# Kernel tuning notes

Measured on AMD Instinct MI355X. Metric: run time of the kernel, lower is better.

## Reference

```python
import jax, jax.numpy as jnp
import numpy as np

HEADS = 16
DIM_HEAD = 128
SCALE = DIM_HEAD ** -0.5


def rotate_half(x):
    # x: (..., d) with d even; pairs (x1, x2) -> (-x2, x1)
    x = x.reshape(*x.shape[:-1], -1, 2)
    x1, x2 = x[..., 0], x[..., 1]
    return jnp.stack([-x2, x1], axis=-1).reshape(*x.shape[:-2], -1)


def apply_rotary(freqs, t):
    # freqs: (n, d), t: (b, h, n, d)
    cos = jnp.cos(freqs)[None, None]
    sin = jnp.sin(freqs)[None, None]
    return t * cos + rotate_half(t) * sin


def setup_inputs() -> dict:
    key = jax.random.key(0)
    ks = jax.random.split(key, 6)
    b, n, dim = 2, 2048, 2048
    inner = HEADS * DIM_HEAD
    s = dim ** -0.5
    x = jax.random.normal(ks[0], (b, n, dim), dtype=jnp.float32)
    rotary_emb = jax.random.normal(ks[1], (n, DIM_HEAD), dtype=jnp.float32)
    Wq = jax.random.normal(ks[2], (dim, inner), dtype=jnp.float32) * s
    Wkv = jax.random.normal(ks[3], (dim, 2 * inner), dtype=jnp.float32) * s
    Wo = jax.random.normal(ks[4], (inner, dim), dtype=jnp.float32) * s
    bo = jnp.zeros((dim,), dtype=jnp.float32)
    return {"x": x, "rotary_emb": rotary_emb, "Wq": Wq, "Wkv": Wkv, "Wo": Wo, "bo": bo}


def reference(x, rotary_emb, Wq, Wkv, Wo, bo):
    b, n, _ = x.shape
    q = x @ Wq                      # (b, n, inner)
    kv = x @ Wkv                    # (b, n, 2*inner)
    k, v = jnp.split(kv, 2, axis=-1)
    # b n (h d) -> b h n d
    split = lambda t: t.reshape(b, n, HEADS, DIM_HEAD).transpose(0, 2, 1, 3)
    q, k, v = split(q), split(k), split(v)
    q = apply_rotary(rotary_emb, q)
    k = apply_rotary(rotary_emb, k)
    q = q * SCALE
    dots = jnp.einsum('bhid,bhjd->bhij', q, k)
    attn = jax.nn.softmax(dots, axis=-1)
    out = jnp.einsum('bhij,bhjd->bhid', attn, v)
    out = out.transpose(0, 2, 1, 3).reshape(b, n, HEADS * DIM_HEAD)
    return out @ Wo + bo
```

## Files before the change

kernel.cpp:

```cpp
#include <hip/hip_runtime.h>
#include <hip/hip_bf16.h>
#include <stdint.h>

typedef __attribute__((ext_vector_type(8))) short s16x8;
typedef __attribute__((ext_vector_type(4))) float f32x4;

#define DEVFN static __device__ __forceinline__

constexpr int   S_LEN = 2048;
constexpr int   DH    = 128;
constexpr int   INNER = 2048;
constexpr float ASCALE = 0.08838834764831845f;

constexpr float SM_L2E  = 1.44269504f;
constexpr float SM_BIAS = 12.0f * 1.44269504f;

DEVFN unsigned short f2b(float f) {
  union { __hip_bfloat16 h; unsigned short u; } v;
  v.h = __float2bfloat16(f);
  return v.u;
}
DEVFN void async_cp16(const unsigned short* g, unsigned short* l) {
  __builtin_amdgcn_global_load_lds((const __attribute__((address_space(1))) void*)g,
                                   (__attribute__((address_space(3))) void*)l, 16, 0, 0);
}

__global__ __launch_bounds__(256) void cvt_bf16_k(const float* __restrict__ in,
                                                  unsigned short* __restrict__ out) {
  const size_t e = ((size_t)blockIdx.x * 256 + threadIdx.x) * 8;
  const float4 a = *(const float4*)(in + e);
  const float4 b = *(const float4*)(in + e + 4);
  union { s16x8 v; unsigned short u[8]; } o;
  o.u[0] = f2b(a.x); o.u[1] = f2b(a.y); o.u[2] = f2b(a.z); o.u[3] = f2b(a.w);
  o.u[4] = f2b(b.x); o.u[5] = f2b(b.y); o.u[6] = f2b(b.z); o.u[7] = f2b(b.w);
  *(s16x8*)(out + e) = o.v;
}

__global__ __launch_bounds__(256) void rot_cs_k(const float* __restrict__ rot,
                                                float2* __restrict__ cst) {
  const int idx = blockIdx.x * 256 + threadIdx.x;
  const float f = rot[idx];
  float s, c;
  __sincosf(f, &s, &c);
  cst[idx] = make_float2(c, s);
}

__global__ __launch_bounds__(256) void transpose_cvt_k(const float* __restrict__ in,
                                                       unsigned short* __restrict__ out,
                                                       int R, int C) {
  __shared__ __align__(16) unsigned short tile[64][72];
  const int t  = threadIdx.x;
  const int lr = t >> 3;
  const int lc = (t & 7) << 3;
  const size_t ibase = (size_t)blockIdx.y * 64 * C + (size_t)blockIdx.x * 64;
#pragma unroll
  for (int rr = 0; rr < 64; rr += 32) {
    const float* p = in + ibase + (size_t)(rr + lr) * C + lc;
    const float4 a = *(const float4*)p;
    const float4 b = *(const float4*)(p + 4);
    unsigned short* tp = &tile[rr + lr][lc];
    tp[0] = f2b(a.x); tp[1] = f2b(a.y); tp[2] = f2b(a.z); tp[3] = f2b(a.w);
    tp[4] = f2b(b.x); tp[5] = f2b(b.y); tp[6] = f2b(b.z); tp[7] = f2b(b.w);
  }
  __syncthreads();
  const size_t obase = (size_t)blockIdx.x * 64 * R + (size_t)blockIdx.y * 64;
#pragma unroll
  for (int rr = 0; rr < 64; rr += 32) {
    int oc = rr + lr;
    union { s16x8 v; unsigned short s[8]; } u;
#pragma unroll
    for (int j = 0; j < 8; ++j) u.s[j] = tile[lc + j][oc];
    *(s16x8*)(out + obase + (size_t)oc * R + lc) = u.v;
  }
}

__global__ __launch_bounds__(512, 2) void gemm256_qk(
    const unsigned short* __restrict__ A,
    const unsigned short* __restrict__ Bt,
    unsigned short* __restrict__ out0,
    unsigned short* __restrict__ out1,
    const float2* __restrict__ rotcs) {
  constexpr int K = 2048, NT = 32;
  __shared__ __align__(16) unsigned short smem[65536];
  const int tid = threadIdx.x;
  const int wid = tid >> 6, lane = tid & 63;
  const int wm = wid >> 2, wn = wid & 3;
  const int quad = lane >> 4, l15 = lane & 15, l7 = l15 & 7;

  const int lin = blockIdx.x;
  const int logical = (lin & 7) * 32 + (lin >> 3);
  const int m0 = (logical & 15) * 256;
  const int n0 = (logical >> 4) * 256;

  const int r0 = tid >> 3, c0 = tid & 7;

  f32x4 acc[8][4];
#pragma unroll
  for (int i = 0; i < 8; ++i)
#pragma unroll
    for (int j = 0; j < 4; ++j) acc[i][j] = {0.f, 0.f, 0.f, 0.f};

  auto stageA = [&](int t, int h) {
#pragma unroll
    for (int s = 0; s < 2; ++s) {
      const int r = s * 64 + r0;
      async_cp16(A + (size_t)(m0 + h * 128 + r) * K + t * 64 + ((c0 ^ (r0 & 7)) << 3),
                 smem + ((t & 1) * 2 + h) * 8192 + s * 4096 + tid * 8);
    }
  };
  auto stageB = [&](int t, int h) {
#pragma unroll
    for (int s = 0; s < 2; ++s) {
      const int r = s * 64 + r0;
      async_cp16(Bt + (size_t)(n0 + h * 128 + r) * K + t * 64 + ((c0 ^ (r0 & 7)) << 3),
                 smem + 32768 + ((t & 1) * 2 + h) * 8192 + s * 4096 + tid * 8);
    }
  };

  stageA(0, 0); stageA(0, 1); stageB(0, 0); stageB(0, 1);
  stageB(1, 0); stageB(1, 1);
  asm volatile("s_waitcnt vmcnt(4)" ::: "memory");
  __builtin_amdgcn_s_barrier();

#pragma unroll 2
  for (int t = 0; t < NT; ++t) {
    const int cur = t & 1;
    const unsigned short* Ab = smem + (cur * 2 + wm) * 8192;
    const unsigned short* Bb = smem + 32768 + (cur * 2 + (wn >> 1)) * 8192;
    const int bln = (wn & 1) * 64;
    s16x8 bf[4][2];
#pragma unroll
    for (int p = 0; p < 2; ++p) {
      s16x8 af[2][2];
#pragma unroll
      for (int j = 0; j < 2; ++j)
#pragma unroll
        for (int kk = 0; kk < 2; ++kk)
          af[j][kk] = *(const s16x8*)(Ab + ((4 * p + j) * 16 + l15) * 64 + (((kk * 4 + quad) ^ l7) << 3));
      if (p == 0) {
#pragma unroll
        for (int nf = 0; nf < 4; ++nf)
#pragma unroll
          for (int kk = 0; kk < 2; ++kk)
            bf[nf][kk] = *(const s16x8*)(Bb + (bln + nf * 16 + l15) * 64 + (((kk * 4 + quad) ^ l7) << 3));
        if (t + 1 < NT) { stageA(t + 1, 0); stageA(t + 1, 1); }
      } else {
        if (t + 2 < NT) { stageB(t + 2, 0); stageB(t + 2, 1); }
      }
      __builtin_amdgcn_s_barrier();
      asm volatile("s_waitcnt lgkmcnt(0)" ::: "memory");
      s16x8 ag[2][2];
#pragma unroll
      for (int j = 0; j < 2; ++j)
#pragma unroll
        for (int kk = 0; kk < 2; ++kk)
          ag[j][kk] = *(const s16x8*)(Ab + ((4 * p + 2 + j) * 16 + l15) * 64 + (((kk * 4 + quad) ^ l7) << 3));
      __builtin_amdgcn_sched_barrier(0);
      __builtin_amdgcn_s_setprio(1);
#pragma unroll
      for (int kk = 0; kk < 2; ++kk)
#pragma unroll
        for (int j = 0; j < 2; ++j)
#pragma unroll
          for (int nf = 0; nf < 4; ++nf)
            acc[4 * p + j][nf] = __builtin_amdgcn_mfma_f32_16x16x32_bf16(af[j][kk], bf[nf][kk], acc[4 * p + j][nf], 0, 0, 0);
      __builtin_amdgcn_s_setprio(0);
      asm volatile("s_waitcnt lgkmcnt(0)" ::: "memory");
      __builtin_amdgcn_sched_barrier(0);
      __builtin_amdgcn_s_setprio(1);
#pragma unroll
      for (int kk = 0; kk < 2; ++kk)
#pragma unroll
        for (int j = 0; j < 2; ++j)
#pragma unroll
          for (int nf = 0; nf < 4; ++nf)
            acc[4 * p + 2 + j][nf] = __builtin_amdgcn_mfma_f32_16x16x32_bf16(ag[j][kk], bf[nf][kk], acc[4 * p + 2 + j][nf], 0, 0, 0);
      __builtin_amdgcn_s_setprio(0);
      __builtin_amdgcn_sched_barrier(0);
      if (p == 1) {
        if (t == NT - 2)      asm volatile("s_waitcnt vmcnt(0)" ::: "memory");
        else if (t < NT - 2)  asm volatile("s_waitcnt vmcnt(4)" ::: "memory");
      }
      __builtin_amdgcn_s_barrier();
    }
  }

  __syncthreads();
  const int b = m0 >> 11, ibase = m0 & 2047;
  const bool isq = (n0 < INNER);
  const int hbase = (n0 & (INNER - 1)) >> 7;
#pragma unroll
  for (int mf = 0; mf < 8; ++mf)
#pragma unroll
    for (int nf = 0; nf < 4; ++nf) {
      const int jl = wn * 64 + nf * 16 + l15;
      const int dd = jl & 127;
      const int cl = jl >> 3;
#pragma unroll
      for (int r = 0; r < 4; ++r) {
        const int il = wm * 128 + mf * 16 + quad * 4 + r;
        const float v  = acc[mf][nf][r];
        const float vp = __shfl_xor(v, 1);
        const float2 cs = rotcs[(size_t)(ibase + il) * 128 + dd];
        float rv = (dd & 1) ? fmaf(v, cs.x,  vp * cs.y)
                            : fmaf(v, cs.x, -vp * cs.y);
        if (isq) rv *= ASCALE;
        smem[il * 256 + ((cl ^ (il & 7)) << 3) + (jl & 7)] = f2b(rv);
      }
    }
  __syncthreads();
  unsigned short* outp = (isq ? out0 : out1) +
                         ((size_t)((b << 4) + hbase) * S_LEN + ibase) * DH;
#pragma unroll
  for (int it = 0; it < 16; ++it) {
    const int f  = it * 512 + tid;
    const int il = f >> 5, cl = f & 31;
    s16x8 vv = *(const s16x8*)(smem + il * 256 + ((cl ^ (il & 7)) << 3));
    const int hh = cl >> 4, dd0 = (cl & 15) << 3;
    *(s16x8*)(outp + (size_t)hh * S_LEN * DH + (size_t)il * DH + dd0) = vv;
  }
}

template <int EPI>
__global__ __launch_bounds__(256) void gemm_bt(
    const unsigned short* __restrict__ A,
    const unsigned short* __restrict__ Bt,
    unsigned short* __restrict__ out2,
    float* __restrict__ outf,
    const float* __restrict__ biasf,
    int M, int N, int K) {
  __shared__ __align__(16) unsigned short smem[16384];
  unsigned short* As = smem;
  unsigned short* Bs = smem + 8192;
  const int tid  = threadIdx.x;
  const int wave = tid >> 6, lane = tid & 63;
  const int wm = wave & 1, wn = wave >> 1;
  const int quad = lane >> 4, l15 = lane & 15;
  const int l7 = l15 & 7;
  const int m0 = blockIdx.x * 128, n0 = blockIdx.y * 128;

  f32x4 acc[4][4];
#pragma unroll
  for (int i = 0; i < 4; ++i)
#pragma unroll
    for (int j = 0; j < 4; ++j) acc[i][j] = {0.f, 0.f, 0.f, 0.f};

  const int lrow = lane >> 3;
  const int lchk = (lane & 7) ^ (lrow & 7);
  const unsigned short* a_g = A  + (size_t)(m0 + wave * 32 + lrow) * K + (lchk << 3);
  const unsigned short* b_g = Bt + (size_t)(n0 + wave * 32 + lrow) * K + (lchk << 3);
  unsigned short* As_w = As + (wave * 32) * 64;
  unsigned short* Bs_w = Bs + (wave * 32) * 64;

  for (int k0 = 0; k0 < K; k0 += 64) {
    __syncthreads();
#pragma unroll
    for (int t = 0; t < 4; ++t) {
      async_cp16(a_g + k0 + (size_t)(t * 8) * K, As_w + t * 8 * 64);
      async_cp16(b_g + k0 + (size_t)(t * 8) * K, Bs_w + t * 8 * 64);
    }
    __syncthreads();
#pragma unroll
    for (int ks = 0; ks < 2; ++ks) {
      s16x8 af[4], bfr[4];
#pragma unroll
      for (int mi = 0; mi < 4; ++mi)
        af[mi] = *(const s16x8*)(As + (wm * 64 + mi * 16 + l15) * 64 + (((ks * 4 + quad) ^ l7) << 3));
#pragma unroll
      for (int ni = 0; ni < 4; ++ni)
        bfr[ni] = *(const s16x8*)(Bs + (wn * 64 + ni * 16 + l15) * 64 + (((ks * 4 + quad) ^ l7) << 3));
#pragma unroll
      for (int mi = 0; mi < 4; ++mi)
#pragma unroll
        for (int ni = 0; ni < 4; ++ni)
          acc[mi][ni] = __builtin_amdgcn_mfma_f32_16x16x32_bf16(af[mi], bfr[ni], acc[mi][ni], 0, 0, 0);
    }
  }

  if constexpr (EPI == 1) {
#pragma unroll
    for (int mi = 0; mi < 4; ++mi)
#pragma unroll
      for (int ni = 0; ni < 4; ++ni)
#pragma unroll
        for (int r = 0; r < 4; ++r) {
          const int gm = m0 + wm * 64 + mi * 16 + quad * 4 + r;
          const int gn = n0 + wn * 64 + ni * 16 + l15;
          outf[(size_t)gm * N + gn] = acc[mi][ni][r] + biasf[gn];
        }
  } else {
    __syncthreads();
    const int b = m0 >> 11, ibase = m0 & 2047;
    const int h = n0 >> 7;
#pragma unroll
    for (int mi = 0; mi < 4; ++mi)
#pragma unroll
      for (int ni = 0; ni < 4; ++ni) {
        const int dd = wn * 64 + ni * 16 + l15;
#pragma unroll
        for (int r = 0; r < 4; ++r) {
          const int il = wm * 64 + mi * 16 + quad * 4 + r;
          smem[dd * 128 + (((il >> 3) ^ (dd & 7)) << 3) + (il & 7)] = f2b(acc[mi][ni][r]);
        }
      }
    __syncthreads();
    unsigned short* outp = out2 + (size_t)((b << 4) + h) * DH * S_LEN + ibase;
#pragma unroll
    for (int it = 0; it < 8; ++it) {
      const int f  = it * 256 + tid;
      const int dd = f >> 4, ch = f & 15;
      s16x8 vv = *(const s16x8*)(smem + dd * 128 + ((ch ^ (dd & 7)) << 3));
      *(s16x8*)(outp + (size_t)dd * S_LEN + (ch << 3)) = vv;
    }
  }
}

DEVFN void stage_tile(const unsigned short* kh, const unsigned short* vh,
                      int j0, unsigned short* KsB, unsigned short* VsB, int tid) {
#pragma unroll
  for (int v = 0; v < 4; ++v) {
    const int off = v * 2048 + tid * 8;
    const int kr = off >> 7;
    const int kc = (((off & 127) >> 3) ^ (kr & 7)) << 3;
    async_cp16(kh + (size_t)(j0 + kr) * DH + kc, KsB + off);
    const int vr = off >> 6;
    const int vc = (((off & 63) >> 3) ^ (vr & 7)) << 3;
    async_cp16(vh + (size_t)vr * S_LEN + j0 + vc, VsB + off);
  }
}

__global__ __launch_bounds__(256, 2) void flash_attn(
    const unsigned short* __restrict__ q,
    const unsigned short* __restrict__ k,
    const unsigned short* __restrict__ vt,
    unsigned short* __restrict__ aout) {
  __shared__ __align__(16) unsigned short Ks[2][64 * 128];
  __shared__ __align__(16) unsigned short Vs[2][128 * 64];
  __shared__ __align__(16) unsigned short Ps[4][32 * 64];
  const int tid = threadIdx.x;
  const int w = tid >> 6, lane = tid & 63;
  const int quad = lane >> 4, l15 = lane & 15;
  const int l7 = l15 & 7;

  const int lin  = blockIdx.y * 16 + blockIdx.x;
  const int xcd  = lin & 7, slot = lin >> 3;
  const int bh   = (xcd << 2) + (slot >> 4);
  const int i0   = (slot & 15) * 128;

  const unsigned short* qh = q  + (size_t)bh * S_LEN * DH;
  const unsigned short* kh = k  + (size_t)bh * S_LEN * DH;
  const unsigned short* vh = vt + (size_t)bh * DH * S_LEN;

  s16x8 qf[2][4];
#pragma unroll
  for (int mi = 0; mi < 2; ++mi)
#pragma unroll
    for (int ks = 0; ks < 4; ++ks)
      qf[mi][ks] = *(const s16x8*)(qh + (size_t)(i0 + w * 32 + mi * 16 + l15) * DH + ks * 32 + quad * 8);

  f32x4 oacc[2][8];
#pragma unroll
  for (int mi = 0; mi < 2; ++mi)
#pragma unroll
    for (int ni = 0; ni < 8; ++ni) oacc[mi][ni] = {0.f, 0.f, 0.f, 0.f};
  float lrun[2][4];
#pragma unroll
  for (int mi = 0; mi < 2; ++mi)
#pragma unroll
    for (int r = 0; r < 4; ++r) lrun[mi][r] = 0.f;

  unsigned short* Pw = Ps[w];

  stage_tile(kh, vh, 0, Ks[0], Vs[0], tid);
  __syncthreads();
  int cur = 0;

  for (int j0 = 0; j0 < S_LEN; j0 += 64) {
    if (j0 + 64 < S_LEN)
      stage_tile(kh, vh, j0 + 64, Ks[cur ^ 1], Vs[cur ^ 1], tid);
    const unsigned short* Ksc = Ks[cur];
    const unsigned short* Vsc = Vs[cur];

    f32x4 sacc[2][4];
#pragma unroll
    for (int mi = 0; mi < 2; ++mi)
#pragma unroll
      for (int ni = 0; ni < 4; ++ni) sacc[mi][ni] = {0.f, 0.f, 0.f, 0.f};
    __builtin_amdgcn_s_setprio(1);
#pragma unroll
    for (int ks = 0; ks < 4; ++ks) {
      s16x8 kb[4];
#pragma unroll
      for (int ni = 0; ni < 4; ++ni)
        kb[ni] = *(const s16x8*)(Ksc + (ni * 16 + l15) * 128 + (((ks * 4 + quad) ^ l7) << 3));
#pragma unroll
      for (int mi = 0; mi < 2; ++mi)
#pragma unroll
        for (int ni = 0; ni < 4; ++ni)
          sacc[mi][ni] = __builtin_amdgcn_mfma_f32_16x16x32_bf16(qf[mi][ks], kb[ni], sacc[mi][ni], 0, 0, 0);
    }
    __builtin_amdgcn_s_setprio(0);

#pragma unroll
    for (int mi = 0; mi < 2; ++mi)
#pragma unroll
      for (int r = 0; r < 4; ++r) {
        float s0 = 0.f;
#pragma unroll
        for (int ni = 0; ni < 4; ++ni) {
          float p = __builtin_amdgcn_exp2f(fmaf(sacc[mi][ni][r], SM_L2E, -SM_BIAS));
          sacc[mi][ni][r] = p;
          s0 += p;
        }
        lrun[mi][r] += s0;
      }

#pragma unroll
    for (int mi = 0; mi < 2; ++mi)
#pragma unroll
      for (int ni = 0; ni < 2; ++ni) {
        const int col = ni * 16 + l15;
        const int ch  = col >> 3;
#pragma unroll
        for (int r = 0; r < 4; ++r) {
          const int row = mi * 16 + quad * 4 + r;
          Pw[row * 64 + ((ch ^ (row & 7)) << 3) + (col & 7)] = f2b(sacc[mi][ni][r]);
        }
      }
    asm volatile("s_waitcnt lgkmcnt(0)" ::: "memory");
    __builtin_amdgcn_sched_barrier(0);
    {
      const int swz = (quad ^ l7) << 3;
      s16x8 pf[2];
#pragma unroll
      for (int mi = 0; mi < 2; ++mi)
        pf[mi] = *(const s16x8*)(Pw + (mi * 16 + l15) * 64 + swz);
      __builtin_amdgcn_s_setprio(1);
#pragma unroll
      for (int ni = 0; ni < 8; ++ni) {
        s16x8 vb = *(const s16x8*)(Vsc + (ni * 16 + l15) * 64 + swz);
#pragma unroll
        for (int mi = 0; mi < 2; ++mi)
          oacc[mi][ni] = __builtin_amdgcn_mfma_f32_16x16x32_bf16(pf[mi], vb, oacc[mi][ni], 0, 0, 0);
      }
      __builtin_amdgcn_s_setprio(0);
    }

#pragma unroll
    for (int mi = 0; mi < 2; ++mi)
#pragma unroll
      for (int ni = 2; ni < 4; ++ni) {
        const int col = ni * 16 + l15;
        const int ch  = col >> 3;
#pragma unroll
        for (int r = 0; r < 4; ++r) {
          const int row = mi * 16 + quad * 4 + r;
          Pw[row * 64 + ((ch ^ (row & 7)) << 3) + (col & 7)] = f2b(sacc[mi][ni][r]);
        }
      }
    asm volatile("s_waitcnt lgkmcnt(0)" ::: "memory");
    __builtin_amdgcn_sched_barrier(0);
    {
      const int swz = ((4 + quad) ^ l7) << 3;
      s16x8 pf[2];
#pragma unroll
      for (int mi = 0; mi < 2; ++mi)
        pf[mi] = *(const s16x8*)(Pw + (mi * 16 + l15) * 64 + swz);
      __builtin_amdgcn_s_setprio(1);
#pragma unroll
      for (int ni = 0; ni < 8; ++ni) {
        s16x8 vb = *(const s16x8*)(Vsc + (ni * 16 + l15) * 64 + swz);
#pragma unroll
        for (int mi = 0; mi < 2; ++mi)
          oacc[mi][ni] = __builtin_amdgcn_mfma_f32_16x16x32_bf16(pf[mi], vb, oacc[mi][ni], 0, 0, 0);
      }
      __builtin_amdgcn_s_setprio(0);
    }

    __syncthreads();
    cur ^= 1;
  }

  const int b = bh >> 4, h = bh & 15;
#pragma unroll
  for (int mi = 0; mi < 2; ++mi)
#pragma unroll
    for (int r = 0; r < 4; ++r) {
      float l = lrun[mi][r];
      l += __shfl_xor(l, 1);
      l += __shfl_xor(l, 2);
      l += __shfl_xor(l, 4);
      l += __shfl_xor(l, 8);
      const float inv = 1.0f / l;
      const int i = i0 + w * 32 + mi * 16 + quad * 4 + r;
#pragma unroll
      for (int ni = 0; ni < 8; ++ni) {
        const int dd = ni * 16 + l15;
        aout[((size_t)b * S_LEN + i) * INNER + h * DH + dd] = f2b(oacc[mi][ni][r] * inv);
      }
    }
}

extern "C" void kernel_launch(void* const* d_in, const int* in_sizes, int n_in,
                              void* d_out, int out_size, void* d_ws, size_t ws_size,
                              hipStream_t stream) {
  const float* x   = (const float*)d_in[0];
  const float* rot = (const float*)d_in[1];
  const float* Wq  = (const float*)d_in[2];
  const float* Wkv = (const float*)d_in[3];
  const float* Wo  = (const float*)d_in[4];
  const float* bo  = (const float*)d_in[5];
  float* out = (float*)d_out;

  unsigned short* ws = (unsigned short*)d_ws;
  unsigned short* wt  = ws;
  unsigned short* wot = wt  + (size_t)6144 * 2048;
  unsigned short* qb  = wot + (size_t)2048 * 2048;
  unsigned short* kb  = qb  + (size_t)32 * 2048 * 128;
  unsigned short* vtb = kb  + (size_t)32 * 2048 * 128;
  unsigned short* xb  = vtb + (size_t)32 * 2048 * 128;
  unsigned short* att = wt;

  float2* cst = (float2*)d_out;

  rot_cs_k<<<dim3(1024), 256, 0, stream>>>(rot, cst);
  cvt_bf16_k<<<dim3(4096), 256, 0, stream>>>(x, xb);
  transpose_cvt_k<<<dim3(32, 32), 256, 0, stream>>>(Wq,  wt, 2048, 2048);
  transpose_cvt_k<<<dim3(64, 32), 256, 0, stream>>>(Wkv, wt + (size_t)2048 * 2048, 2048, 4096);
  transpose_cvt_k<<<dim3(32, 32), 256, 0, stream>>>(Wo,  wot, 2048, 2048);

  gemm256_qk<<<dim3(256), 512, 0, stream>>>(xb, wt, qb, kb, cst);
  gemm_bt<2><<<dim3(32, 16), 256, 0, stream>>>(xb, wt + (size_t)4096 * 2048, vtb,
                                               nullptr, nullptr, 4096, 2048, 2048);
  flash_attn<<<dim3(16, 32), 256, 0, stream>>>(qb, kb, vtb, att);
  gemm_bt<1><<<dim3(32, 16), 256, 0, stream>>>(att, wot, nullptr, out, bo, 4096, 2048, 2048);
}
```

Before: 380.8 us.

## Replace 128x128 GEMM with pipelined 128x256 tile GEMM and simplify attention PV loop

The V-projection and output-projection GEMMs move from a 128x128 tile kernel with 4 waves, which synchronised twice per K step, to a 128x256 tile kernel with 8 waves. The new kernel double-buffers A and triple-buffers B using async global-to-LDS loads, interleaving prefetch with MFMA work through explicit vmcnt waits and barriers. Separately, the flash-attention inner loop now writes the whole P tile before its two PV half-steps and drops the s_setprio hints. The aim is better latency hiding and more reuse per block in the GEMMs, at the cost of much larger LDS use (128KB per block) and more complex synchronisation.

```diff
diff --git a/kernel.cpp b/kernel.cpp
--- a/kernel.cpp
+++ b/kernel.cpp
@@ -222,22 +222,24 @@
 }
 
 template <int EPI>
-__global__ __launch_bounds__(256) void gemm_bt(
+__global__ __launch_bounds__(512, 2) void gemm128x256(
     const unsigned short* __restrict__ A,
     const unsigned short* __restrict__ Bt,
     unsigned short* __restrict__ out2,
     float* __restrict__ outf,
-    const float* __restrict__ biasf,
-    int M, int N, int K) {
-  __shared__ __align__(16) unsigned short smem[16384];
-  unsigned short* As = smem;
-  unsigned short* Bs = smem + 8192;
-  const int tid  = threadIdx.x;
-  const int wave = tid >> 6, lane = tid & 63;
-  const int wm = wave & 1, wn = wave >> 1;
-  const int quad = lane >> 4, l15 = lane & 15;
-  const int l7 = l15 & 7;
-  const int m0 = blockIdx.x * 128, n0 = blockIdx.y * 128;
+    const float* __restrict__ biasf) {
+  constexpr int K = 2048, NT = 32, N = 2048;
+  __shared__ __align__(16) unsigned short smem[65536];
+  const int tid = threadIdx.x;
+  const int wid = tid >> 6, lane = tid & 63;
+  const int wm = wid >> 2, wn = wid & 3;
+  const int quad = lane >> 4, l15 = lane & 15, l7 = l15 & 7;
+
+  const int lin = blockIdx.x;
+  const int n0 = (lin & 7) * 256;
+  const int m0 = (lin >> 3) * 128;
+
+  const int r0 = tid >> 3, c0 = tid & 7;
 
   f32x4 acc[4][4];
 #pragma unroll
@@ -245,35 +247,64 @@
 #pragma unroll
     for (int j = 0; j < 4; ++j) acc[i][j] = {0.f, 0.f, 0.f, 0.f};
 
-  const int lrow = lane >> 3;
-  const int lchk = (lane & 7) ^ (lrow & 7);
-  const unsigned short* a_g = A  + (size_t)(m0 + wave * 32 + lrow) * K + (lchk << 3);
-  const unsigned short* b_g = Bt + (size_t)(n0 + wave * 32 + lrow) * K + (lchk << 3);
-  unsigned short* As_w = As + (wave * 32) * 64;
-  unsigned short* Bs_w = Bs + (wave * 32) * 64;
-
-  for (int k0 = 0; k0 < K; k0 += 64) {
-    __syncthreads();
-#pragma unroll
-    for (int t = 0; t < 4; ++t) {
-      async_cp16(a_g + k0 + (size_t)(t * 8) * K, As_w + t * 8 * 64);
-      async_cp16(b_g + k0 + (size_t)(t * 8) * K, Bs_w + t * 8 * 64);
-    }
-    __syncthreads();
-#pragma unroll
-    for (int ks = 0; ks < 2; ++ks) {
-      s16x8 af[4], bfr[4];
-#pragma unroll
-      for (int mi = 0; mi < 4; ++mi)
-        af[mi] = *(const s16x8*)(As + (wm * 64 + mi * 16 + l15) * 64 + (((ks * 4 + quad) ^ l7) << 3));
-#pragma unroll
-      for (int ni = 0; ni < 4; ++ni)
-        bfr[ni] = *(const s16x8*)(Bs + (wn * 64 + ni * 16 + l15) * 64 + (((ks * 4 + quad) ^ l7) << 3));
-#pragma unroll
-      for (int mi = 0; mi < 4; ++mi)
-#pragma unroll
-        for (int ni = 0; ni < 4; ++ni)
-          acc[mi][ni] = __builtin_amdgcn_mfma_f32_16x16x32_bf16(af[mi], bfr[ni], acc[mi][ni], 0, 0, 0);
+  auto stageA = [&](int t) {
+#pragma unroll
+    for (int s = 0; s < 2; ++s)
+      async_cp16(A + (size_t)(m0 + s * 64 + r0) * K + t * 64 + ((c0 ^ (r0 & 7)) << 3),
+                 smem + (t & 1) * 8192 + s * 4096 + tid * 8);
+  };
+  auto stageB = [&](int t) {
+    const int bs = 16384 + (t % 3) * 16384;
+#pragma unroll
+    for (int s = 0; s < 4; ++s)
+      async_cp16(Bt + (size_t)(n0 + s * 64 + r0) * K + t * 64 + ((c0 ^ (r0 & 7)) << 3),
+                 smem + bs + s * 4096 + tid * 8);
+  };
+
+  stageA(0); stageB(0); stageB(1);
+  asm volatile("s_waitcnt vmcnt(4)" ::: "memory");
+  __builtin_amdgcn_s_barrier();
+
+  for (int t = 0; t < NT; ++t) {
+    const unsigned short* Ab = smem + (t & 1) * 8192;
+    const unsigned short* Bb = smem + 16384 + (t % 3) * 16384;
+    s16x8 bf[4][2];
+#pragma unroll
+    for (int p = 0; p < 2; ++p) {
+      s16x8 af[2][2];
+#pragma unroll
+      for (int j = 0; j < 2; ++j)
+#pragma unroll
+        for (int kk = 0; kk < 2; ++kk)
+          af[j][kk] = *(const s16x8*)(Ab + (wm * 64 + (2 * p + j) * 16 + l15) * 64 + (((kk * 4 + quad) ^ l7) << 3));
+      if (p == 0) {
+#pragma unroll
+        for (int nf = 0; nf < 4; ++nf)
+#pragma unroll
+          for (int kk = 0; kk < 2; ++kk)
+            bf[nf][kk] = *(const s16x8*)(Bb + (wn * 64 + nf * 16 + l15) * 64 + (((kk * 4 + quad) ^ l7) << 3));
+        if (t + 1 < NT) stageA(t + 1);
+      } else {
+        if (t + 2 < NT) stageB(t + 2);
+      }
+      __builtin_amdgcn_s_barrier();
+      asm volatile("s_waitcnt lgkmcnt(0)" ::: "memory");
+      __builtin_amdgcn_sched_barrier(0);
+      __builtin_amdgcn_s_setprio(1);
+#pragma unroll
+      for (int kk = 0; kk < 2; ++kk)
+#pragma unroll
+        for (int j = 0; j < 2; ++j)
+#pragma unroll
+          for (int nf = 0; nf < 4; ++nf)
+            acc[2 * p + j][nf] = __builtin_amdgcn_mfma_f32_16x16x32_bf16(af[j][kk], bf[nf][kk], acc[2 * p + j][nf], 0, 0, 0);
+      __builtin_amdgcn_s_setprio(0);
+      __builtin_amdgcn_sched_barrier(0);
+      if (p == 1) {
+        if (t == NT - 2)      asm volatile("s_waitcnt vmcnt(0)" ::: "memory");
+        else if (t < NT - 2)  asm volatile("s_waitcnt vmcnt(4)" ::: "memory");
+      }
+      __builtin_amdgcn_s_barrier();
     }
   }
 
@@ -281,36 +312,36 @@
 #pragma unroll
     for (int mi = 0; mi < 4; ++mi)
 #pragma unroll
-      for (int ni = 0; ni < 4; ++ni)
+      for (int nf = 0; nf < 4; ++nf)
 #pragma unroll
         for (int r = 0; r < 4; ++r) {
           const int gm = m0 + wm * 64 + mi * 16 + quad * 4 + r;
-          const int gn = n0 + wn * 64 + ni * 16 + l15;
-          outf[(size_t)gm * N + gn] = acc[mi][ni][r] + biasf[gn];
+          const int gn = n0 + wn * 64 + nf * 16 + l15;
+          outf[(size_t)gm * N + gn] = acc[mi][nf][r] + biasf[gn];
         }
   } else {
     __syncthreads();
     const int b = m0 >> 11, ibase = m0 & 2047;
-    const int h = n0 >> 7;
 #pragma unroll
     for (int mi = 0; mi < 4; ++mi)
 #pragma unroll
-      for (int ni = 0; ni < 4; ++ni) {
-        const int dd = wn * 64 + ni * 16 + l15;
+      for (int nf = 0; nf < 4; ++nf) {
+        const int jl = wn * 64 + nf * 16 + l15;
 #pragma unroll
         for (int r = 0; r < 4; ++r) {
           const int il = wm * 64 + mi * 16 + quad * 4 + r;
-          smem[dd * 128 + (((il >> 3) ^ (dd & 7)) << 3) + (il & 7)] = f2b(acc[mi][ni][r]);
+          smem[jl * 128 + (((il >> 3) ^ (jl & 7)) << 3) + (il & 7)] = f2b(acc[mi][nf][r]);
         }
       }
     __syncthreads();
-    unsigned short* outp = out2 + (size_t)((b << 4) + h) * DH * S_LEN + ibase;
+    unsigned short* outp = out2 + (size_t)(b << 4) * DH * S_LEN + ibase;
 #pragma unroll
     for (int it = 0; it < 8; ++it) {
-      const int f  = it * 256 + tid;
-      const int dd = f >> 4, ch = f & 15;
-      s16x8 vv = *(const s16x8*)(smem + dd * 128 + ((ch ^ (dd & 7)) << 3));
-      *(s16x8*)(outp + (size_t)dd * S_LEN + (ch << 3)) = vv;
+      const int f  = it * 512 + tid;
+      const int jl = f >> 4, ch = f & 15;
+      s16x8 vv = *(const s16x8*)(smem + jl * 128 + ((ch ^ (jl & 7)) << 3));
+      const int head = (n0 >> 7) + (jl >> 7), dd = jl & 127;
+      *(s16x8*)(outp + ((size_t)head * DH + dd) * S_LEN + (ch << 3)) = vv;
     }
   }
 }
@@ -386,7 +417,6 @@
     for (int mi = 0; mi < 2; ++mi)
 #pragma unroll
       for (int ni = 0; ni < 4; ++ni) sacc[mi][ni] = {0.f, 0.f, 0.f, 0.f};
-    __builtin_amdgcn_s_setprio(1);
 #pragma unroll
     for (int ks = 0; ks < 4; ++ks) {
       s16x8 kb[4];
@@ -399,7 +429,6 @@
         for (int ni = 0; ni < 4; ++ni)
           sacc[mi][ni] = __builtin_amdgcn_mfma_f32_16x16x32_bf16(qf[mi][ks], kb[ni], sacc[mi][ni], 0, 0, 0);
     }
-    __builtin_amdgcn_s_setprio(0);
 
 #pragma unroll
     for (int mi = 0; mi < 2; ++mi)
@@ -418,7 +447,7 @@
 #pragma unroll
     for (int mi = 0; mi < 2; ++mi)
 #pragma unroll
-      for (int ni = 0; ni < 2; ++ni) {
+      for (int ni = 0; ni < 4; ++ni) {
         const int col = ni * 16 + l15;
         const int ch  = col >> 3;
 #pragma unroll
@@ -427,15 +456,15 @@
           Pw[row * 64 + ((ch ^ (row & 7)) << 3) + (col & 7)] = f2b(sacc[mi][ni][r]);
         }
       }
-    asm volatile("s_waitcnt lgkmcnt(0)" ::: "memory");
-    __builtin_amdgcn_sched_barrier(0);
-    {
-      const int swz = (quad ^ l7) << 3;
+    __threadfence_block();
+
+#pragma unroll
+    for (int ks = 0; ks < 2; ++ks) {
+      const int swz = ((ks * 4 + quad) ^ l7) << 3;
       s16x8 pf[2];
 #pragma unroll
       for (int mi = 0; mi < 2; ++mi)
         pf[mi] = *(const s16x8*)(Pw + (mi * 16 + l15) * 64 + swz);
-      __builtin_amdgcn_s_setprio(1);
 #pragma unroll
       for (int ni = 0; ni < 8; ++ni) {
         s16x8 vb = *(const s16x8*)(Vsc + (ni * 16 + l15) * 64 + swz);
@@ -443,38 +472,6 @@
         for (int mi = 0; mi < 2; ++mi)
           oacc[mi][ni] = __builtin_amdgcn_mfma_f32_16x16x32_bf16(pf[mi], vb, oacc[mi][ni], 0, 0, 0);
       }
-      __builtin_amdgcn_s_setprio(0);
-    }
-
-#pragma unroll
-    for (int mi = 0; mi < 2; ++mi)
-#pragma unroll
-      for (int ni = 2; ni < 4; ++ni) {
-        const int col = ni * 16 + l15;
-        const int ch  = col >> 3;
-#pragma unroll
-        for (int r = 0; r < 4; ++r) {
-          const int row = mi * 16 + quad * 4 + r;
-          Pw[row * 64 + ((ch ^ (row & 7)) << 3) + (col & 7)] = f2b(sacc[mi][ni][r]);
-        }
-      }
-    asm volatile("s_waitcnt lgkmcnt(0)" ::: "memory");
-    __builtin_amdgcn_sched_barrier(0);
-    {
-      const int swz = ((4 + quad) ^ l7) << 3;
-      s16x8 pf[2];
-#pragma unroll
-      for (int mi = 0; mi < 2; ++mi)
-        pf[mi] = *(const s16x8*)(Pw + (mi * 16 + l15) * 64 + swz);
-      __builtin_amdgcn_s_setprio(1);
-#pragma unroll
-      for (int ni = 0; ni < 8; ++ni) {
-        s16x8 vb = *(const s16x8*)(Vsc + (ni * 16 + l15) * 64 + swz);
-#pragma unroll
-        for (int mi = 0; mi < 2; ++mi)
-          oacc[mi][ni] = __builtin_amdgcn_mfma_f32_16x16x32_bf16(pf[mi], vb, oacc[mi][ni], 0, 0, 0);
-      }
-      __builtin_amdgcn_s_setprio(0);
     }
 
     __syncthreads();
@@ -530,8 +527,8 @@
   transpose_cvt_k<<<dim3(32, 32), 256, 0, stream>>>(Wo,  wot, 2048, 2048);
 
   gemm256_qk<<<dim3(256), 512, 0, stream>>>(xb, wt, qb, kb, cst);
-  gemm_bt<2><<<dim3(32, 16), 256, 0, stream>>>(xb, wt + (size_t)4096 * 2048, vtb,
-                                               nullptr, nullptr, 4096, 2048, 2048);
+  gemm128x256<2><<<dim3(256), 512, 0, stream>>>(xb, wt + (size_t)4096 * 2048, vtb,
+                                                nullptr, nullptr);
   flash_attn<<<dim3(16, 32), 256, 0, stream>>>(qb, kb, vtb, att);
-  gemm_bt<1><<<dim3(32, 16), 256, 0, stream>>>(att, wot, nullptr, out, bo, 4096, 2048, 2048);
-}
+  gemm128x256<1><<<dim3(256), 512, 0, stream>>>(att, wot, nullptr, out, bo);
+}
```

Result: no change. 385.4 us (+1.2%).
